# Kernel tuning notes

Hardware: AMD Instinct MI355X
Metric: run time of the kernel (lower is better)

## Reference

```python
import jax, jax.numpy as jnp
import numpy as np

B, N, DIM = 32, 576, 1024
H, HD = 16, 64            # head_dim = DIM // H
M = HD * 2                # rand_feat_dim = head_dim * rand_feat_dim_ratio(2) = 128
LAM = 0.1
NUM_STEP = 10
SCALE = HD ** (-0.5)


def setup_inputs() -> dict:
    key = jax.random.key(0)
    ks = jax.random.split(key, 6)
    x = jax.random.normal(ks[0], (B, N, DIM), dtype=jnp.float32)
    qkv_w = jax.random.normal(ks[1], (2 * DIM, DIM), dtype=jnp.float32) * 0.02
    proj_w = jax.random.normal(ks[2], (DIM, DIM), dtype=jnp.float32) * 0.02
    proj_b = jnp.zeros((DIM,), dtype=jnp.float32)
    rand_matrix = jax.random.normal(ks[3], (H, HD, M), dtype=jnp.float32)
    kernel = jax.random.normal(ks[4], (1, H, N, M), dtype=jnp.float32)
    learned_k = jnp.eye(2 * M, dtype=jnp.float32)
    learned_lam = jnp.ones((1,), dtype=jnp.float32)
    learned_L = jnp.ones((1,), dtype=jnp.float32)
    return {"x": x, "qkv_w": qkv_w, "proj_w": proj_w, "proj_b": proj_b,
            "rand_matrix": rand_matrix, "kernel": kernel,
            "learned_k": learned_k, "learned_lam": learned_lam,
            "learned_L": learned_L}


def _soft_thresh(z, t):
    # torch: sign(z) * GELU(|z| - t), exact (erf) GELU
    return jnp.sign(z) * jax.nn.gelu(jnp.abs(z) - t, approximate=False)


def reference(x, qkv_w, proj_w, proj_b, rand_matrix, kernel,
              learned_k, learned_lam, learned_L):
    # qkv projection (no bias), split into q and v heads: [B,H,N,HD]
    qkv = (x @ qkv_w.T).reshape(B, N, 2, H, HD)
    q = jnp.transpose(qkv[:, :, 0], (0, 2, 1, 3))
    v = jnp.transpose(qkv[:, :, 1], (0, 2, 1, 3))

    # random-feature map (Performer-style positive features)
    q = q * SCALE ** 0.5
    logits = jnp.einsum('bhnd,hdm->bhnm', q, rand_matrix)
    sqnorm = 0.5 * jnp.sum(q * q, axis=-1, keepdims=True)
    phi = jnp.exp(logits - sqnorm) / (M ** 0.5)                 # [B,H,N,M]

    # concat learned kernel features, L2-normalize over token dim (dim=-2)
    q = jnp.concatenate([phi, jnp.broadcast_to(kernel, (B, H, N, M))], axis=-1)
    nrm = jnp.linalg.norm(q, axis=-2, keepdims=True)
    q = q / jnp.maximum(nrm, 1e-12)                              # [B,H,N,2M]

    kk = jnp.einsum('bhnp,bhnq->bhpq', q, q)                     # [B,H,2M,2M]
    inp = jnp.einsum('bhnp,bhnd->bhpd', q, v)                    # [B,H,2M,HD]

    # ISTA-like unrolled solver
    L = jax.lax.stop_gradient(
        jnp.max(jnp.sum(jnp.abs(kk), axis=-1), axis=-1))[..., None, None] + 1.0
    lam_learned = learned_lam * LAM                              # [1]
    eff_L = L / learned_L                                        # [B,H,1,1]
    kk_learned = jnp.einsum('pq,bhqr,rs->bhps', learned_k, kk, learned_k)

    z = _soft_thresh(inp, lam_learned)
    for _ in range(NUM_STEP):
        z = z - (jnp.einsum('bhpq,bhqd->bhpd', kk_learned, z) - inp) / eff_L
        z = _soft_thresh(z, lam_learned / eff_L)

    out = jnp.einsum('bhnp,bhpd->bhnd', q, z)                    # [B,H,N,HD]
    out = jnp.transpose(out, (0, 2, 1, 3)).reshape(B, N, DIM)
    return out @ proj_w.T + proj_b
```

## Files before the change

kernel.cpp:

```cpp
#include <hip/hip_runtime.h>
#include <math.h>

#define NN 576
#define LAMC 0.1f
#define NUM_STEP 10

typedef unsigned short u16;
typedef __attribute__((ext_vector_type(8))) short bf16x8;
typedef __attribute__((ext_vector_type(4))) float f32x4;

__device__ __forceinline__ float bf2f(u16 u) { return __uint_as_float(((unsigned)u) << 16); }
__device__ __forceinline__ u16 f2bf(float f) {
    unsigned x = __float_as_uint(f);
    return (u16)((x + 0x7fffu + ((x >> 16) & 1u)) >> 16);
}
__device__ __forceinline__ float soft_thresh(float z, float t) {
    float a = fabsf(z) - t;
    float g = 0.5f * a * (1.0f + erff(a * 0.70710678118654752f));
    float s = (z > 0.0f) ? 1.0f : ((z < 0.0f) ? -1.0f : 0.0f);
    return s * g;
}
__device__ __forceinline__ void gload16(const u16* g, const u16* l) {
    __builtin_amdgcn_global_load_lds(
        (const __attribute__((address_space(1))) unsigned int*)(g),
        (__attribute__((address_space(3))) unsigned int*)(l), 16, 0, 0);
}

__global__ __launch_bounds__(256) void k_prep(const float* __restrict__ x,
                                              const float* __restrict__ qkv_w,
                                              const float* __restrict__ proj_w,
                                              const float* __restrict__ Lk,
                                              const float* __restrict__ rand_m,
                                              const float* __restrict__ kern,
                                              u16* __restrict__ xb,
                                              u16* __restrict__ wb,
                                              u16* __restrict__ pwb,
                                              u16* __restrict__ Lkb,
                                              u16* __restrict__ LkTb,
                                              u16* __restrict__ randT,
                                              u16* __restrict__ kerT) {
    const int b = blockIdx.x;
    if (b < 18432) {
        const int i = b * 256 + threadIdx.x;
        float4 v = reinterpret_cast<const float4*>(x)[i];
        ushort4 o; o.x = f2bf(v.x); o.y = f2bf(v.y); o.z = f2bf(v.z); o.w = f2bf(v.w);
        reinterpret_cast<ushort4*>(xb)[i] = o;
    } else if (b < 20480) {
        const int i = (b - 18432) * 256 + threadIdx.x;
        float4 v = reinterpret_cast<const float4*>(qkv_w)[i];
        ushort4 o; o.x = f2bf(v.x); o.y = f2bf(v.y); o.z = f2bf(v.z); o.w = f2bf(v.w);
        reinterpret_cast<ushort4*>(wb)[i] = o;
    } else if (b < 21504) {
        const int i = (b - 20480) * 256 + threadIdx.x;
        float4 v = reinterpret_cast<const float4*>(proj_w)[i];
        ushort4 o; o.x = f2bf(v.x); o.y = f2bf(v.y); o.z = f2bf(v.z); o.w = f2bf(v.w);
        reinterpret_cast<ushort4*>(pwb)[i] = o;
    } else if (b < 21568) {
        const int i = (b - 21504) * 256 + threadIdx.x;
        float4 v = reinterpret_cast<const float4*>(Lk)[i];
        ushort4 o; o.x = f2bf(v.x); o.y = f2bf(v.y); o.z = f2bf(v.z); o.w = f2bf(v.w);
        reinterpret_cast<ushort4*>(Lkb)[i] = o;
    } else if (b < 21824) {
        const int r = b - 21568, s = threadIdx.x;
        LkTb[r * 256 + s] = f2bf(Lk[s * 256 + r]);
    } else if (b < 22336) {
        const int i = (b - 21824) * 256 + threadIdx.x;
        const int h = i >> 13, rem = i & 8191;
        const int m = rem >> 6, d = rem & 63;
        randT[i] = f2bf(rand_m[(size_t)h * 8192 + d * 128 + m]);
    } else {
        const int h = b - 22336, m = threadIdx.x;
        if (m < 128) {
            const float* kp = kern + (size_t)h * NN * 128 + m;
            float s = 0.f;
            for (int n = 0; n < NN; ++n) { float v = kp[(size_t)n * 128]; s = fmaf(v, v, s); }
            const float inv = 1.0f / fmaxf(sqrtf(s), 1e-12f);
            u16* op = kerT + ((size_t)h * 128 + m) * 576;
            for (int n = 0; n < NN; ++n) op[n] = f2bf(kp[(size_t)n * 128] * inv);
        }
    }
}

__device__ __forceinline__ void nt128_k64(const u16* __restrict__ A, const u16* __restrict__ B,
                                          const int K, u16 (&As)[128][64], u16 (&Bs)[128][64],
                                          f32x4 (&acc)[4][4]) {
    const int tid = threadIdx.x;
    const int lane = tid & 63, wid = tid >> 6;
    const int wr = (wid >> 1) * 64, wc = (wid & 1) * 64;
    const int fr = lane & 15, kg = lane >> 4;
    const int lrow = lane >> 3;
    const int lslot = (lane & 7) ^ ((lane >> 3) & 7);
    for (int k0 = 0; k0 < K; k0 += 64) {
        __syncthreads();
        #pragma unroll
        for (int c = 0; c < 4; ++c) {
            const int ch = wid + c * 4;
            gload16(&A[(size_t)(ch * 8 + lrow) * K + k0 + lslot * 8], &As[ch * 8][0]);
            gload16(&B[(size_t)(ch * 8 + lrow) * K + k0 + lslot * 8], &Bs[ch * 8][0]);
        }
        __syncthreads();
        #pragma unroll
        for (int ks = 0; ks < 2; ++ks) {
            const int rs = ((ks * 4 + kg) ^ (fr & 7)) * 8;
            bf16x8 af[4], bfr[4];
            #pragma unroll
            for (int i = 0; i < 4; ++i) af[i] = *reinterpret_cast<const bf16x8*>(&As[wr + i * 16 + fr][rs]);
            #pragma unroll
            for (int j = 0; j < 4; ++j) bfr[j] = *reinterpret_cast<const bf16x8*>(&Bs[wc + j * 16 + fr][rs]);
            #pragma unroll
            for (int i = 0; i < 4; ++i)
                #pragma unroll
                for (int j = 0; j < 4; ++j)
                    acc[i][j] = __builtin_amdgcn_mfma_f32_16x16x32_bf16(af[i], bfr[j], acc[i][j], 0, 0, 0);
        }
    }
}

__global__ __launch_bounds__(256) void k_qkv_mfma(const u16* __restrict__ A,
                                                  const u16* __restrict__ B,
                                                  u16* __restrict__ qbf,
                                                  u16* __restrict__ vT) {
    __shared__ u16 As[128][64];
    __shared__ u16 Bs[128][64];
    const int tid = threadIdx.x;
    const int wid = tid >> 6, lane = tid & 63;
    const int wr = (wid >> 1) * 64, wc = (wid & 1) * 64;
    const int lb = (blockIdx.x & 7) * 288 + (blockIdx.x >> 3);
    const int bm = lb >> 4, bn = lb & 15;
    const int row0 = bm * 128, col0 = bn * 128;
    const int fr = lane & 15, kg = lane >> 4;
    f32x4 acc[4][4];
    #pragma unroll
    for (int i = 0; i < 4; ++i)
        #pragma unroll
        for (int j = 0; j < 4; ++j) acc[i][j] = (f32x4){0.f, 0.f, 0.f, 0.f};
    nt128_k64(A + (size_t)row0 * 1024, B + (size_t)col0 * 1024, 1024, As, Bs, acc);
    const bool isQ = (col0 < 1024);
    if (isQ) {
        const float qscale = 0.35355339059327373f;
        #pragma unroll
        for (int i = 0; i < 4; ++i) {
            #pragma unroll
            for (int r = 0; r < 4; ++r) {
                const int grow = row0 + wr + i * 16 + kg * 4 + r;
                const int b = grow / NN, n = grow % NN;
                #pragma unroll
                for (int j = 0; j < 4; ++j) {
                    const int gcol = col0 + wc + j * 16 + fr;
                    const int h = gcol >> 6, d = gcol & 63;
                    qbf[(((size_t)b * 16 + h) * NN + n) * 64 + d] = f2bf(acc[i][j][r] * qscale);
                }
            }
        }
    } else {
        #pragma unroll
        for (int i = 0; i < 4; ++i) {
            const int gb = row0 + wr + i * 16 + kg * 4;
            const int b = gb / NN, n = gb % NN;
            #pragma unroll
            for (int j = 0; j < 4; ++j) {
                const int c2 = col0 + wc + j * 16 + fr - 1024;
                const int h = c2 >> 6, d = c2 & 63;
                ushort4 pk;
                pk.x = f2bf(acc[i][j][0]); pk.y = f2bf(acc[i][j][1]);
                pk.z = f2bf(acc[i][j][2]); pk.w = f2bf(acc[i][j][3]);
                *reinterpret_cast<ushort4*>(&vT[(((size_t)b * 16 + h) * 64 + d) * 576 + n]) = pk;
            }
        }
    }
}

__global__ __launch_bounds__(256) void k_phi_mfma(const u16* __restrict__ qbf,
                                                  const u16* __restrict__ randT,
                                                  u16* __restrict__ phiT,
                                                  float* __restrict__ invn) {
    __shared__ u16 Rs[128][72];
    __shared__ u16 Qs[64][72];
    __shared__ u16 Ph[128][72];
    __shared__ float sn[64];
    __shared__ float snorm[256];
    const int bh = blockIdx.x, h = bh & 15;
    const int tid = threadIdx.x, lane = tid & 63, wid = tid >> 6;
    const int fr = lane & 15, kg = lane >> 4;
    #pragma unroll
    for (int c = 0; c < 4; ++c) {
        const int i = c * 256 + tid;
        const int m = i >> 3, k8 = (i & 7) * 8;
        *reinterpret_cast<uint4*>(&Rs[m][k8]) =
            *reinterpret_cast<const uint4*>(&randT[((size_t)h * 128 + m) * 64 + k8]);
    }
    const u16* Q = qbf + (size_t)bh * 576 * 64;
    const float invM = 0.08838834764831845f;
    float accs = 0.f;
    const int m2 = tid >> 1, c0 = (tid & 1) * 32;
    for (int nc = 0; nc < 9; ++nc) {
        const int n0 = nc * 64;
        __syncthreads();
        #pragma unroll
        for (int c = 0; c < 2; ++c) {
            const int i = c * 256 + tid;
            const int r = i >> 3, k8 = (i & 7) * 8;
            *reinterpret_cast<uint4*>(&Qs[r][k8]) =
                *reinterpret_cast<const uint4*>(&Q[(size_t)(n0 + r) * 64 + k8]);
        }
        __syncthreads();
        if (tid < 64) {
            float s = 0.f;
            #pragma unroll 8
            for (int d = 0; d < 64; ++d) { float v = bf2f(Qs[tid][d]); s = fmaf(v, v, s); }
            sn[tid] = 0.5f * s;
        }
        f32x4 acc[2][4];
        #pragma unroll
        for (int i = 0; i < 2; ++i)
            #pragma unroll
            for (int j = 0; j < 4; ++j) acc[i][j] = (f32x4){0.f, 0.f, 0.f, 0.f};
        #pragma unroll
        for (int ks = 0; ks < 2; ++ks) {
            bf16x8 af[2], bq[4];
            #pragma unroll
            for (int i = 0; i < 2; ++i)
                af[i] = *reinterpret_cast<const bf16x8*>(&Rs[wid * 32 + i * 16 + fr][ks * 32 + kg * 8]);
            #pragma unroll
            for (int j = 0; j < 4; ++j)
                bq[j] = *reinterpret_cast<const bf16x8*>(&Qs[j * 16 + fr][ks * 32 + kg * 8]);
            #pragma unroll
            for (int i = 0; i < 2; ++i)
                #pragma unroll
                for (int j = 0; j < 4; ++j)
                    acc[i][j] = __builtin_amdgcn_mfma_f32_16x16x32_bf16(af[i], bq[j], acc[i][j], 0, 0, 0);
        }
        __syncthreads();
        #pragma unroll
        for (int j = 0; j < 4; ++j) {
            const int n = j * 16 + fr;
            const float sv = sn[n];
            #pragma unroll
            for (int i = 0; i < 2; ++i) {
                #pragma unroll
                for (int r = 0; r < 4; ++r) {
                    const int m = wid * 32 + i * 16 + kg * 4 + r;
                    Ph[m][n] = f2bf(expf(acc[i][j][r] - sv) * invM);
                }
            }
        }
        __syncthreads();
        #pragma unroll
        for (int c = 0; c < 4; ++c) {
            const int i = c * 256 + tid;
            const int mm = i >> 3, k8 = (i & 7) * 8;
            *reinterpret_cast<uint4*>(&phiT[((size_t)bh * 128 + mm) * 576 + n0 + k8]) =
                *reinterpret_cast<const uint4*>(&Ph[mm][k8]);
        }
        {
            float s = 0.f;
            #pragma unroll 8
            for (int t = 0; t < 32; ++t) { float v = bf2f(Ph[m2][c0 + t]); s = fmaf(v, v, s); }
            accs += s;
        }
    }
    snorm[tid] = accs;
    __syncthreads();
    if (tid < 128)
        invn[bh * 128 + tid] = 1.0f / fmaxf(sqrtf(snorm[tid * 2] + snorm[tid * 2 + 1]), 1e-12f);
}

__global__ __launch_bounds__(512, 2) void k_gram_fat(const u16* __restrict__ phiT,
                                                     const u16* __restrict__ kerT,
                                                     const float* __restrict__ invn,
                                                     const float* __restrict__ lL,
                                                     u16* __restrict__ kkb,
                                                     float* __restrict__ effL) {
    __shared__ u16 Qs[256][64];
    __shared__ float rs2[2][256];
    __shared__ float red[256];
    const int bh = blockIdx.x, h = bh & 15;
    const int tid = threadIdx.x, lane = tid & 63, wid = tid >> 6;
    const int wr = (wid & 3) * 64, wc = (wid >> 2) * 128;
    const int fr = lane & 15, kg = lane >> 4;
    const int lrow = lane >> 3;
    const int lslot = (lane & 7) ^ ((lane >> 3) & 7);
    f32x4 acc[4][8];
    #pragma unroll
    for (int i = 0; i < 4; ++i)
        #pragma unroll
        for (int j = 0; j < 8; ++j) acc[i][j] = (f32x4){0.f, 0.f, 0.f, 0.f};
    for (int k0 = 0; k0 < 576; k0 += 64) {
        __syncthreads();
        #pragma unroll
        for (int c = 0; c < 4; ++c) {
            const int rowbase = (wid * 4 + c) * 8;
            const int p = rowbase + lrow;
            const u16* src = (p < 128)
                ? phiT + ((size_t)bh * 128 + p) * 576 + k0 + lslot * 8
                : kerT + ((size_t)h * 128 + (p - 128)) * 576 + k0 + lslot * 8;
            gload16(src, &Qs[rowbase][0]);
        }
        __syncthreads();
        #pragma unroll
        for (int ks = 0; ks < 2; ++ks) {
            const int rs = ((ks * 4 + kg) ^ (fr & 7)) * 8;
            bf16x8 af[4], bf[8];
            #pragma unroll
            for (int i = 0; i < 4; ++i) af[i] = *reinterpret_cast<const bf16x8*>(&Qs[wr + i * 16 + fr][rs]);
            #pragma unroll
            for (int j = 0; j < 8; ++j) bf[j] = *reinterpret_cast<const bf16x8*>(&Qs[wc + j * 16 + fr][rs]);
            #pragma unroll
            for (int i = 0; i < 4; ++i)
                #pragma unroll
                for (int j = 0; j < 8; ++j)
                    acc[i][j] = __builtin_amdgcn_mfma_f32_16x16x32_bf16(af[i], bf[j], acc[i][j], 0, 0, 0);
        }
    }
    const float* iv = invn + bh * 128;
    u16* C = kkb + (size_t)bh * 65536;
    float sq[8];
    #pragma unroll
    for (int j = 0; j < 8; ++j) { const int q = wc + j * 16 + fr; sq[j] = (q < 128) ? iv[q] : 1.0f; }
    #pragma unroll
    for (int i = 0; i < 4; ++i)
        #pragma unroll
        for (int rr = 0; rr < 4; ++rr) {
            const int p = wr + i * 16 + kg * 4 + rr;
            const float sp = (p < 128) ? iv[p] : 1.0f;
            float rsum = 0.f;
            #pragma unroll
            for (int j = 0; j < 8; ++j) {
                const float val = acc[i][j][rr] * sp * sq[j];
                C[(size_t)p * 256 + wc + j * 16 + fr] = f2bf(val);
                rsum += fabsf(val);
            }
            #pragma unroll
            for (int mk = 1; mk < 16; mk <<= 1) rsum += __shfl_xor(rsum, mk);
            if (fr == 0) rs2[wid >> 2][p] = rsum;
        }
    __syncthreads();
    if (tid < 256) red[tid] = rs2[0][tid] + rs2[1][tid];
    __syncthreads();
    for (int st = 128; st > 0; st >>= 1) {
        if (tid < st) red[tid] = fmaxf(red[tid], red[tid + st]);
        __syncthreads();
    }
    if (tid == 0) effL[bh] = (red[0] + 1.0f) / lL[0];
}

__global__ __launch_bounds__(512, 2) void k_lk_fat(const u16* __restrict__ Ab, size_t sA,
                                                   const u16* __restrict__ Bb, size_t sB,
                                                   u16* __restrict__ Cb) {
    __shared__ u16 As[256][64];
    __shared__ u16 Bs[256][64];
    const int idx = blockIdx.x;
    const int tid = threadIdx.x, lane = tid & 63, wid = tid >> 6;
    const int wr = (wid & 3) * 64, wc = (wid >> 2) * 128;
    const int fr = lane & 15, kg = lane >> 4;
    const int lrow = lane >> 3;
    const int lslot = (lane & 7) ^ ((lane >> 3) & 7);
    const u16* A = Ab + (size_t)idx * sA;
    const u16* B = Bb + (size_t)idx * sB;
    f32x4 acc[4][8];
    #pragma unroll
    for (int i = 0; i < 4; ++i)
        #pragma unroll
        for (int j = 0; j < 8; ++j) acc[i][j] = (f32x4){0.f, 0.f, 0.f, 0.f};
    for (int k0 = 0; k0 < 256; k0 += 64) {
        __syncthreads();
        #pragma unroll
        for (int c = 0; c < 4; ++c) {
            const int rowbase = (wid * 4 + c) * 8;
            const int p = rowbase + lrow;
            gload16(&A[(size_t)p * 256 + k0 + lslot * 8], &As[rowbase][0]);
            gload16(&B[(size_t)p * 256 + k0 + lslot * 8], &Bs[rowbase][0]);
        }
        __syncthreads();
        #pragma unroll
        for (int ks = 0; ks < 2; ++ks) {
            const int rs = ((ks * 4 + kg) ^ (fr & 7)) * 8;
            bf16x8 af[4], bf[8];
            #pragma unroll
            for (int i = 0; i < 4; ++i) af[i] = *reinterpret_cast<const bf16x8*>(&As[wr + i * 16 + fr][rs]);
            #pragma unroll
            for (int j = 0; j < 8; ++j) bf[j] = *reinterpret_cast<const bf16x8*>(&Bs[wc + j * 16 + fr][rs]);
            #pragma unroll
            for (int i = 0; i < 4; ++i)
                #pragma unroll
                for (int j = 0; j < 8; ++j)
                    acc[i][j] = __builtin_amdgcn_mfma_f32_16x16x32_bf16(af[i], bf[j], acc[i][j], 0, 0, 0);
        }
    }
    u16* C = Cb + (size_t)idx * 65536;
    #pragma unroll
    for (int i = 0; i < 4; ++i)
        #pragma unroll
        for (int rr = 0; rr < 4; ++rr) {
            const int p = wr + i * 16 + kg * 4 + rr;
            #pragma unroll
            for (int j = 0; j < 8; ++j)
                C[(size_t)p * 256 + wc + j * 16 + fr] = f2bf(acc[i][j][rr]);
        }
}

__global__ __launch_bounds__(256) void k_inp_mfma(const u16* __restrict__ vT,
                                                  const u16* __restrict__ phiT,
                                                  const u16* __restrict__ kerT,
                                                  const float* __restrict__ invn,
                                                  float* __restrict__ inpT) {
    __shared__ u16 As[64][32];
    __shared__ u16 Bs[256][32];
    const int bh = blockIdx.x, h = bh & 15;
    const int tid = threadIdx.x, lane = tid & 63, wid = tid >> 6;
    const int fr = lane & 15, kg = lane >> 4;
    const int lrow = lane >> 2;
    const int lslot = (lane & 3) ^ ((lane >> 3) & 3);
    const u16* Av = vT + (size_t)bh * 64 * 576;
    f32x4 acc[4][4];
    #pragma unroll
    for (int i = 0; i < 4; ++i)
        #pragma unroll
        for (int j = 0; j < 4; ++j) acc[i][j] = (f32x4){0.f, 0.f, 0.f, 0.f};
    const int rslot = (kg ^ ((fr >> 1) & 3)) * 8;
    for (int k0 = 0; k0 < 576; k0 += 32) {
        __syncthreads();
        gload16(&Av[(size_t)(wid * 16 + lrow) * 576 + k0 + lslot * 8], &As[wid * 16][0]);
        #pragma unroll
        for (int c = 0; c < 4; ++c) {
            const int chunk = wid + c * 4;
            const int p = chunk * 16 + lrow;
            const u16* src = (p < 128)
                ? phiT + ((size_t)bh * 128 + p) * 576 + k0 + lslot * 8
                : kerT + ((size_t)h * 128 + (p - 128)) * 576 + k0 + lslot * 8;
            gload16(src, &Bs[chunk * 16][0]);
        }
        __syncthreads();
        bf16x8 af[4], bfr[4];
        #pragma unroll
        for (int i = 0; i < 4; ++i) af[i] = *reinterpret_cast<const bf16x8*>(&As[i * 16 + fr][rslot]);
        #pragma unroll
        for (int j = 0; j < 4; ++j) bfr[j] = *reinterpret_cast<const bf16x8*>(&Bs[wid * 64 + j * 16 + fr][rslot]);
        #pragma unroll
        for (int i = 0; i < 4; ++i)
            #pragma unroll
            for (int j = 0; j < 4; ++j)
                acc[i][j] = __builtin_amdgcn_mfma_f32_16x16x32_bf16(af[i], bfr[j], acc[i][j], 0, 0, 0);
    }
    float* O = inpT + (size_t)bh * 16384;
    float sc[4];
    #pragma unroll
    for (int j = 0; j < 4; ++j) {
        const int p = wid * 64 + j * 16 + fr;
        sc[j] = (p < 128) ? invn[bh * 128 + p] : 1.0f;
    }
    #pragma unroll
    for (int i = 0; i < 4; ++i)
        #pragma unroll
        for (int r = 0; r < 4; ++r)
            #pragma unroll
            for (int j = 0; j < 4; ++j)
                O[(size_t)(i * 16 + kg * 4 + r) * 256 + wid * 64 + j * 16 + fr] = acc[i][j][r] * sc[j];
}

__global__ __launch_bounds__(256) void k_ista_reg(const u16* __restrict__ kkl,
                                                  const float* __restrict__ inpT,
                                                  u16* __restrict__ zbf,
                                                  const float* __restrict__ effL,
                                                  const float* __restrict__ llam) {
    __shared__ u16 zs[32][256];
    const int lb = (blockIdx.x & 7) * 128 + (blockIdx.x >> 3);
    const int bh = lb >> 1, dh = lb & 1;
    const int tid = threadIdx.x, lane = tid & 63, wid = tid >> 6;
    const int wr = wid * 64;
    const int fr = lane & 15, kg = lane >> 4;
    const u16* Kk = kkl + (size_t)bh * 65536;
    bf16x8 af[4][8];
    #pragma unroll
    for (int i = 0; i < 4; ++i) {
        const int p = wr + i * 16 + fr;
        #pragma unroll
        for (int c = 0; c < 8; ++c)
            af[i][c] = *reinterpret_cast<const bf16x8*>(&Kk[(size_t)p * 256 + c * 32 + kg * 8]);
    }
    const float* I = inpT + (size_t)bh * 16384 + (size_t)dh * 32 * 256;
    const float invL = 1.0f / effL[bh];
    const float lam = llam[0] * LAMC;
    const float thr = lam * invL;
    float4 ip[4][2];
    #pragma unroll
    for (int i = 0; i < 4; ++i) {
        const int pb = wr + i * 16 + kg * 4;
        #pragma unroll
        for (int j = 0; j < 2; ++j) {
            const int d = j * 16 + fr;
            ip[i][j] = *reinterpret_cast<const float4*>(&I[(size_t)d * 256 + pb]);
            const int pc = pb ^ ((d & 7) << 3);
            ushort4 pk;
            pk.x = f2bf(soft_thresh(ip[i][j].x, lam));
            pk.y = f2bf(soft_thresh(ip[i][j].y, lam));
            pk.z = f2bf(soft_thresh(ip[i][j].z, lam));
            pk.w = f2bf(soft_thresh(ip[i][j].w, lam));
            *reinterpret_cast<ushort4*>(&zs[d][pc]) = pk;
        }
    }
    __syncthreads();
    for (int step = 0; step < NUM_STEP; ++step) {
        f32x4 acc[4][2];
        #pragma unroll
        for (int i = 0; i < 4; ++i)
            #pragma unroll
            for (int j = 0; j < 2; ++j) acc[i][j] = (f32x4){0.f, 0.f, 0.f, 0.f};
        #pragma unroll
        for (int c = 0; c < 8; ++c) {
            bf16x8 bz[2];
            #pragma unroll
            for (int j = 0; j < 2; ++j) {
                const int d = j * 16 + fr;
                bz[j] = *reinterpret_cast<const bf16x8*>(&zs[d][(c * 32 + kg * 8) ^ ((d & 7) << 3)]);
            }
            #pragma unroll
            for (int i = 0; i < 4; ++i)
                #pragma unroll
                for (int j = 0; j < 2; ++j)
                    acc[i][j] = __builtin_amdgcn_mfma_f32_16x16x32_bf16(af[i][c], bz[j], acc[i][j], 0, 0, 0);
        }
        __syncthreads();
        #pragma unroll
        for (int i = 0; i < 4; ++i) {
            const int pb = wr + i * 16 + kg * 4;
            #pragma unroll
            for (int j = 0; j < 2; ++j) {
                const int d = j * 16 + fr;
                const int pc = pb ^ ((d & 7) << 3);
                ushort4 zo = *reinterpret_cast<const ushort4*>(&zs[d][pc]);
                ushort4 pk;
                pk.x = f2bf(soft_thresh(bf2f(zo.x) - (acc[i][j][0] - ip[i][j].x) * invL, thr));
                pk.y = f2bf(soft_thresh(bf2f(zo.y) - (acc[i][j][1] - ip[i][j].y) * invL, thr));
                pk.z = f2bf(soft_thresh(bf2f(zo.z) - (acc[i][j][2] - ip[i][j].z) * invL, thr));
                pk.w = f2bf(soft_thresh(bf2f(zo.w) - (acc[i][j][3] - ip[i][j].w) * invL, thr));
                *reinterpret_cast<ushort4*>(&zs[d][pc]) = pk;
            }
        }
        __syncthreads();
    }
    u16* Z = zbf + (size_t)bh * 16384 + (size_t)dh * 32 * 256;
    #pragma unroll
    for (int c = 0; c < 4; ++c) {
        const int i = c * 256 + tid;
        const int d = i >> 5, p8 = (i & 31) * 8;
        *reinterpret_cast<uint4*>(&Z[(size_t)d * 256 + p8]) =
            *reinterpret_cast<const uint4*>(&zs[d][p8 ^ ((d & 7) << 3)]);
    }
}

__global__ __launch_bounds__(256) void k_outpre_mfma(const u16* __restrict__ phiT,
                                                     const u16* __restrict__ kerT,
                                                     const u16* __restrict__ zbf,
                                                     const float* __restrict__ invn,
                                                     u16* __restrict__ outp) {
    __shared__ u16 Zs[64][264];
    __shared__ u16 Qt[64][264];
    __shared__ u16 Os[64][72];
    const int bh = blockIdx.x, b = bh >> 4, h = bh & 15;
    const int tid = threadIdx.x, lane = tid & 63, wid = tid >> 6;
    const int fr = lane & 15, kg = lane >> 4;
    const u16* Z = zbf + (size_t)bh * 16384;
    #pragma unroll
    for (int c = 0; c < 8; ++c) {
        const int i = c * 256 + tid;
        const int d = i >> 5, k8 = (i & 31) * 8;
        uint4 v = *reinterpret_cast<const uint4*>(&Z[(size_t)d * 256 + k8]);
        if (k8 < 128) {
            const float4 s0 = *reinterpret_cast<const float4*>(&invn[bh * 128 + k8]);
            const float4 s1 = *reinterpret_cast<const float4*>(&invn[bh * 128 + k8 + 4]);
            uint4 o;
            o.x = (unsigned)f2bf(__uint_as_float(v.x << 16) * s0.x) |
                  ((unsigned)f2bf(__uint_as_float(v.x & 0xffff0000u) * s0.y) << 16);
            o.y = (unsigned)f2bf(__uint_as_float(v.y << 16) * s0.z) |
                  ((unsigned)f2bf(__uint_as_float(v.y & 0xffff0000u) * s0.w) << 16);
            o.z = (unsigned)f2bf(__uint_as_float(v.z << 16) * s1.x) |
                  ((unsigned)f2bf(__uint_as_float(v.z & 0xffff0000u) * s1.y) << 16);
            o.w = (unsigned)f2bf(__uint_as_float(v.w << 16) * s1.z) |
                  ((unsigned)f2bf(__uint_as_float(v.w & 0xffff0000u) * s1.w) << 16);
            v = o;
        }
        *reinterpret_cast<uint4*>(&Zs[d][k8]) = v;
    }
    for (int nc = 0; nc < 9; ++nc) {
        const int n0 = nc * 64;
        __syncthreads();
        #pragma unroll
        for (int c = 0; c < 8; ++c) {
            const int i = c * 256 + tid;
            const int p = i >> 3, j8 = (i & 7) * 8;
            const u16* src = (p < 128) ? &phiT[((size_t)bh * 128 + p) * 576 + n0 + j8]
                                       : &kerT[((size_t)h * 128 + (p - 128)) * 576 + n0 + j8];
            uint4 v = *reinterpret_cast<const uint4*>(src);
            Qt[j8 + 0][p] = (u16)(v.x & 0xffffu); Qt[j8 + 1][p] = (u16)(v.x >> 16);
            Qt[j8 + 2][p] = (u16)(v.y & 0xffffu); Qt[j8 + 3][p] = (u16)(v.y >> 16);
            Qt[j8 + 4][p] = (u16)(v.z & 0xffffu); Qt[j8 + 5][p] = (u16)(v.z >> 16);
            Qt[j8 + 6][p] = (u16)(v.w & 0xffffu); Qt[j8 + 7][p] = (u16)(v.w >> 16);
        }
        __syncthreads();
        f32x4 acc[4];
        #pragma unroll
        for (int j = 0; j < 4; ++j) acc[j] = (f32x4){0.f, 0.f, 0.f, 0.f};
        #pragma unroll
        for (int ks = 0; ks < 8; ++ks) {
            bf16x8 aq = *reinterpret_cast<const bf16x8*>(&Qt[wid * 16 + fr][ks * 32 + kg * 8]);
            #pragma unroll
            for (int j = 0; j < 4; ++j) {
                bf16x8 bz = *reinterpret_cast<const bf16x8*>(&Zs[j * 16 + fr][ks * 32 + kg * 8]);
                acc[j] = __builtin_amdgcn_mfma_f32_16x16x32_bf16(aq, bz, acc[j], 0, 0, 0);
            }
        }
        __syncthreads();
        #pragma unroll
        for (int j = 0; j < 4; ++j)
            #pragma unroll
            for (int r = 0; r < 4; ++r)
                Os[wid * 16 + kg * 4 + r][j * 16 + fr] = f2bf(acc[j][r]);
        __syncthreads();
        #pragma unroll
        for (int c = 0; c < 2; ++c) {
            const int i = c * 256 + tid;
            const int nn = i >> 3, k8 = (i & 7) * 8;
            *reinterpret_cast<uint4*>(&outp[((size_t)b * NN + n0 + nn) * 1024 + h * 64 + k8]) =
                *reinterpret_cast<const uint4*>(&Os[nn][k8]);
        }
    }
}

__global__ __launch_bounds__(256) void k_proj_mfma(const u16* __restrict__ A,
                                                   const u16* __restrict__ B,
                                                   const float* __restrict__ bias,
                                                   float* __restrict__ out) {
    __shared__ u16 As[128][64];
    __shared__ u16 Bs[128][64];
    const int tid = threadIdx.x;
    const int wid = tid >> 6, lane = tid & 63;
    const int wr = (wid >> 1) * 64, wc = (wid & 1) * 64;
    const int lb = (blockIdx.x & 7) * 144 + (blockIdx.x >> 3);
    const int bm = lb >> 3, bn = lb & 7;
    const int row0 = bm * 128, col0 = bn * 128;
    const int fr = lane & 15, kg = lane >> 4;
    f32x4 acc[4][4];
    #pragma unroll
    for (int i = 0; i < 4; ++i)
        #pragma unroll
        for (int j = 0; j < 4; ++j) acc[i][j] = (f32x4){0.f, 0.f, 0.f, 0.f};
    nt128_k64(A + (size_t)row0 * 1024, B + (size_t)col0 * 1024, 1024, As, Bs, acc);
    #pragma unroll
    for (int i = 0; i < 4; ++i)
        #pragma unroll
        for (int r = 0; r < 4; ++r) {
            const int grow = row0 + wr + i * 16 + kg * 4 + r;
            #pragma unroll
            for (int j = 0; j < 4; ++j) {
                const int gcol = col0 + wc + j * 16 + fr;
                out[(size_t)grow * 1024 + gcol] = acc[i][j][r] + bias[gcol];
            }
        }
}

extern "C" void kernel_launch(void* const* d_in, const int* in_sizes, int n_in,
                              void* d_out, int out_size, void* d_ws, size_t ws_size,
                              hipStream_t stream) {
    const float* x      = (const float*)d_in[0];
    const float* qkv_w  = (const float*)d_in[1];
    const float* proj_w = (const float*)d_in[2];
    const float* proj_b = (const float*)d_in[3];
    const float* rand_m = (const float*)d_in[4];
    const float* kern   = (const float*)d_in[5];
    const float* Lk     = (const float*)d_in[6];
    const float* llam   = (const float*)d_in[7];
    const float* lL     = (const float*)d_in[8];
    float* out = (float*)d_out;

    const size_t NEED = 248514560ull;
    if (ws_size < NEED) { hipMemsetAsync(d_out, 0, (size_t)out_size * 4, stream); return; }
    char* base = (char*)d_ws;
    u16*   pwb  = (u16*)  (base + 0);
    float* effL = (float*)(base + 2097152);
    u16*   Lkb  = (u16*)  (base + 2099200);
    u16*   LkTb = (u16*)  (base + 2230272);
    u16*   kerT = (u16*)  (base + 2361344);
    u16*   randT= (u16*)  (base + 4720640);
    u16*   phiT = (u16*)  (base + 4982784);
    u16*   kkb  = (u16*)  (base + 80480256);
    float* inpT = (float*)(base + 147589120);
    u16*   zbf  = (u16*)  (base + 181143552);
    float* invn = (float*)(base + 248252416);
    u16*   vT   = (u16*)  (base + 80480256);
    u16*   wb   = (u16*)  (base + 118228992);
    u16*   qbf  = (u16*)  (base + 147589120);
    u16*   xb   = (u16*)  (base + 197920768);
    u16*   tmpb = (u16*)  (base + 181143552);
    u16*   outp = (u16*)  (base + 80480256);

    k_prep       <<<22352, 256, 0, stream>>>(x, qkv_w, proj_w, Lk, rand_m, kern,
                                             xb, wb, pwb, Lkb, LkTb, randT, kerT);
    k_qkv_mfma   <<<2304,  256, 0, stream>>>(xb, wb, qbf, vT);
    k_phi_mfma   <<<512,   256, 0, stream>>>(qbf, randT, phiT, invn);
    k_inp_mfma   <<<512,   256, 0, stream>>>(vT, phiT, kerT, invn, inpT);
    k_gram_fat   <<<512,   512, 0, stream>>>(phiT, kerT, invn, lL, kkb, effL);
    k_lk_fat     <<<512,   512, 0, stream>>>(Lkb, 0, kkb, 65536, tmpb);
    k_lk_fat     <<<512,   512, 0, stream>>>(tmpb, 65536, LkTb, 0, kkb);
    k_ista_reg   <<<1024,  256, 0, stream>>>(kkb, inpT, zbf, effL, llam);
    k_outpre_mfma<<<512,   256, 0, stream>>>(phiT, kerT, zbf, invn, outp);
    k_proj_mfma  <<<1152,  256, 0, stream>>>(outp, pwb, proj_b, out);
}
```

Before: 571.3 us.

## Fuse the two learned-kernel sandwich GEMMs into one kernel; widen inp K-tile

The two back-to-back k_lk_fat launches computing Lk·kk·LkT are merged into one kernel. The intermediate 256x256 product stays in a swizzled shared-memory tile instead of going through a global temp buffer. This removes one launch and a global round trip per head, at the cost of 144KB LDS per block and occupancy of one block per CU. Separately, k_inp_mfma now uses a K tile of 64 instead of 32, which halves the number of barrier-separated load steps.

```diff
diff --git a/kernel.cpp b/kernel.cpp
--- a/kernel.cpp
+++ b/kernel.cpp
@@ -344,42 +344,91 @@
     if (tid == 0) effL[bh] = (red[0] + 1.0f) / lL[0];
 }
 
-__global__ __launch_bounds__(512, 2) void k_lk_fat(const u16* __restrict__ Ab, size_t sA,
-                                                   const u16* __restrict__ Bb, size_t sB,
-                                                   u16* __restrict__ Cb) {
-    __shared__ u16 As[256][64];
-    __shared__ u16 Bs[256][64];
-    const int idx = blockIdx.x;
+__global__ __launch_bounds__(512, 1) void k_lk_fused(const u16* __restrict__ Lkb,
+                                                     const u16* __restrict__ LkTb,
+                                                     u16* __restrict__ kkb) {
+    __shared__ u16 smem[73728];
+    u16 (*t)[256]  = reinterpret_cast<u16(*)[256]>(smem);
+    u16 (*As1)[64] = reinterpret_cast<u16(*)[64]>(smem);
+    u16 (*Bs1)[64] = reinterpret_cast<u16(*)[64]>(smem + 16384);
+    u16 (*Bs2)[32] = reinterpret_cast<u16(*)[32]>(smem + 65536);
+    const int bh = blockIdx.x;
     const int tid = threadIdx.x, lane = tid & 63, wid = tid >> 6;
     const int wr = (wid & 3) * 64, wc = (wid >> 2) * 128;
     const int fr = lane & 15, kg = lane >> 4;
-    const int lrow = lane >> 3;
-    const int lslot = (lane & 7) ^ ((lane >> 3) & 7);
-    const u16* A = Ab + (size_t)idx * sA;
-    const u16* B = Bb + (size_t)idx * sB;
+    const u16* B1 = kkb + (size_t)bh * 65536;
     f32x4 acc[4][8];
     #pragma unroll
     for (int i = 0; i < 4; ++i)
         #pragma unroll
         for (int j = 0; j < 8; ++j) acc[i][j] = (f32x4){0.f, 0.f, 0.f, 0.f};
-    for (int k0 = 0; k0 < 256; k0 += 64) {
-        __syncthreads();
-        #pragma unroll
-        for (int c = 0; c < 4; ++c) {
-            const int rowbase = (wid * 4 + c) * 8;
-            const int p = rowbase + lrow;
-            gload16(&A[(size_t)p * 256 + k0 + lslot * 8], &As[rowbase][0]);
-            gload16(&B[(size_t)p * 256 + k0 + lslot * 8], &Bs[rowbase][0]);
-        }
-        __syncthreads();
-        #pragma unroll
-        for (int ks = 0; ks < 2; ++ks) {
-            const int rs = ((ks * 4 + kg) ^ (fr & 7)) * 8;
+    {
+        const int lrow = lane >> 3;
+        const int lslot = (lane & 7) ^ ((lane >> 3) & 7);
+        for (int k0 = 0; k0 < 256; k0 += 64) {
+            __syncthreads();
+            #pragma unroll
+            for (int c = 0; c < 4; ++c) {
+                const int rowbase = (wid * 4 + c) * 8;
+                const int p = rowbase + lrow;
+                gload16(&Lkb[(size_t)p * 256 + k0 + lslot * 8], &As1[rowbase][0]);
+                gload16(&B1[(size_t)p * 256 + k0 + lslot * 8], &Bs1[rowbase][0]);
+            }
+            __syncthreads();
+            #pragma unroll
+            for (int ks = 0; ks < 2; ++ks) {
+                const int rs = ((ks * 4 + kg) ^ (fr & 7)) * 8;
+                bf16x8 af[4], bf[8];
+                #pragma unroll
+                for (int i = 0; i < 4; ++i) af[i] = *reinterpret_cast<const bf16x8*>(&As1[wr + i * 16 + fr][rs]);
+                #pragma unroll
+                for (int j = 0; j < 8; ++j) bf[j] = *reinterpret_cast<const bf16x8*>(&Bs1[wc + j * 16 + fr][rs]);
+                #pragma unroll
+                for (int i = 0; i < 4; ++i)
+                    #pragma unroll
+                    for (int j = 0; j < 8; ++j)
+                        acc[i][j] = __builtin_amdgcn_mfma_f32_16x16x32_bf16(af[i], bf[j], acc[i][j], 0, 0, 0);
+            }
+        }
+    }
+    __syncthreads();
+    #pragma unroll
+    for (int i = 0; i < 4; ++i)
+        #pragma unroll
+        for (int rr = 0; rr < 4; ++rr) {
+            const int p = wr + i * 16 + kg * 4 + rr;
+            #pragma unroll
+            for (int j = 0; j < 8; ++j) {
+                const int q = wc + j * 16 + fr;
+                t[p][q ^ ((p & 7) << 3)] = f2bf(acc[i][j][rr]);
+            }
+        }
+    __syncthreads();
+    #pragma unroll
+    for (int i = 0; i < 4; ++i)
+        #pragma unroll
+        for (int j = 0; j < 8; ++j) acc[i][j] = (f32x4){0.f, 0.f, 0.f, 0.f};
+    {
+        const int lrow2 = lane >> 2;
+        const int lslot2 = (lane & 3) ^ ((lane >> 3) & 3);
+        const int rslot2 = (kg ^ ((fr >> 1) & 3)) * 8;
+        for (int k0 = 0; k0 < 256; k0 += 32) {
+            __syncthreads();
+            #pragma unroll
+            for (int c = 0; c < 2; ++c) {
+                const int chunk = wid * 2 + c;
+                const int p = chunk * 16 + lrow2;
+                gload16(&LkTb[(size_t)p * 256 + k0 + lslot2 * 8], &Bs2[chunk * 16][0]);
+            }
+            __syncthreads();
             bf16x8 af[4], bf[8];
             #pragma unroll
-            for (int i = 0; i < 4; ++i) af[i] = *reinterpret_cast<const bf16x8*>(&As[wr + i * 16 + fr][rs]);
-            #pragma unroll
-            for (int j = 0; j < 8; ++j) bf[j] = *reinterpret_cast<const bf16x8*>(&Bs[wc + j * 16 + fr][rs]);
+            for (int i = 0; i < 4; ++i) {
+                const int p = wr + i * 16 + fr;
+                af[i] = *reinterpret_cast<const bf16x8*>(&t[p][(k0 + kg * 8) ^ ((p & 7) << 3)]);
+            }
+            #pragma unroll
+            for (int j = 0; j < 8; ++j) bf[j] = *reinterpret_cast<const bf16x8*>(&Bs2[wc + j * 16 + fr][rslot2]);
             #pragma unroll
             for (int i = 0; i < 4; ++i)
                 #pragma unroll
@@ -387,7 +436,7 @@
                     acc[i][j] = __builtin_amdgcn_mfma_f32_16x16x32_bf16(af[i], bf[j], acc[i][j], 0, 0, 0);
         }
     }
-    u16* C = Cb + (size_t)idx * 65536;
+    u16* C = kkb + (size_t)bh * 65536;
     #pragma unroll
     for (int i = 0; i < 4; ++i)
         #pragma unroll
@@ -404,43 +453,50 @@
                                                   const u16* __restrict__ kerT,
                                                   const float* __restrict__ invn,
                                                   float* __restrict__ inpT) {
-    __shared__ u16 As[64][32];
-    __shared__ u16 Bs[256][32];
+    __shared__ u16 As[64][64];
+    __shared__ u16 Bs[256][64];
     const int bh = blockIdx.x, h = bh & 15;
     const int tid = threadIdx.x, lane = tid & 63, wid = tid >> 6;
     const int fr = lane & 15, kg = lane >> 4;
-    const int lrow = lane >> 2;
-    const int lslot = (lane & 3) ^ ((lane >> 3) & 3);
+    const int lrow = lane >> 3;
+    const int lslot = (lane & 7) ^ ((lane >> 3) & 7);
     const u16* Av = vT + (size_t)bh * 64 * 576;
     f32x4 acc[4][4];
     #pragma unroll
     for (int i = 0; i < 4; ++i)
         #pragma unroll
         for (int j = 0; j < 4; ++j) acc[i][j] = (f32x4){0.f, 0.f, 0.f, 0.f};
-    const int rslot = (kg ^ ((fr >> 1) & 3)) * 8;
-    for (int k0 = 0; k0 < 576; k0 += 32) {
-        __syncthreads();
-        gload16(&Av[(size_t)(wid * 16 + lrow) * 576 + k0 + lslot * 8], &As[wid * 16][0]);
-        #pragma unroll
-        for (int c = 0; c < 4; ++c) {
+    for (int k0 = 0; k0 < 576; k0 += 64) {
+        __syncthreads();
+        #pragma unroll
+        for (int c = 0; c < 2; ++c) {
+            const int chunk = wid * 2 + c;
+            gload16(&Av[(size_t)(chunk * 8 + lrow) * 576 + k0 + lslot * 8], &As[chunk * 8][0]);
+        }
+        #pragma unroll
+        for (int c = 0; c < 8; ++c) {
             const int chunk = wid + c * 4;
-            const int p = chunk * 16 + lrow;
+            const int p = chunk * 8 + lrow;
             const u16* src = (p < 128)
                 ? phiT + ((size_t)bh * 128 + p) * 576 + k0 + lslot * 8
                 : kerT + ((size_t)h * 128 + (p - 128)) * 576 + k0 + lslot * 8;
-            gload16(src, &Bs[chunk * 16][0]);
-        }
-        __syncthreads();
-        bf16x8 af[4], bfr[4];
-        #pragma unroll
-        for (int i = 0; i < 4; ++i) af[i] = *reinterpret_cast<const bf16x8*>(&As[i * 16 + fr][rslot]);
-        #pragma unroll
-        for (int j = 0; j < 4; ++j) bfr[j] = *reinterpret_cast<const bf16x8*>(&Bs[wid * 64 + j * 16 + fr][rslot]);
-        #pragma unroll
-        for (int i = 0; i < 4; ++i)
-            #pragma unroll
-            for (int j = 0; j < 4; ++j)
-                acc[i][j] = __builtin_amdgcn_mfma_f32_16x16x32_bf16(af[i], bfr[j], acc[i][j], 0, 0, 0);
+            gload16(src, &Bs[chunk * 8][0]);
+        }
+        __syncthreads();
+        #pragma unroll
+        for (int ks = 0; ks < 2; ++ks) {
+            const int rs = ((ks * 4 + kg) ^ (fr & 7)) * 8;
+            bf16x8 af[4], bfr[4];
+            #pragma unroll
+            for (int i = 0; i < 4; ++i) af[i] = *reinterpret_cast<const bf16x8*>(&As[i * 16 + fr][rs]);
+            #pragma unroll
+            for (int j = 0; j < 4; ++j) bfr[j] = *reinterpret_cast<const bf16x8*>(&Bs[wid * 64 + j * 16 + fr][rs]);
+            #pragma unroll
+            for (int i = 0; i < 4; ++i)
+                #pragma unroll
+                for (int j = 0; j < 4; ++j)
+                    acc[i][j] = __builtin_amdgcn_mfma_f32_16x16x32_bf16(af[i], bfr[j], acc[i][j], 0, 0, 0);
+        }
     }
     float* O = inpT + (size_t)bh * 16384;
     float sc[4];
@@ -691,7 +747,6 @@
     u16*   wb   = (u16*)  (base + 118228992);
     u16*   qbf  = (u16*)  (base + 147589120);
     u16*   xb   = (u16*)  (base + 197920768);
-    u16*   tmpb = (u16*)  (base + 181143552);
     u16*   outp = (u16*)  (base + 80480256);
 
     k_prep       <<<22352, 256, 0, stream>>>(x, qkv_w, proj_w, Lk, rand_m, kern,
@@ -700,8 +755,7 @@
     k_phi_mfma   <<<512,   256, 0, stream>>>(qbf, randT, phiT, invn);
     k_inp_mfma   <<<512,   256, 0, stream>>>(vT, phiT, kerT, invn, inpT);
     k_gram_fat   <<<512,   512, 0, stream>>>(phiT, kerT, invn, lL, kkb, effL);
-    k_lk_fat     <<<512,   512, 0, stream>>>(Lkb, 0, kkb, 65536, tmpb);
-    k_lk_fat     <<<512,   512, 0, stream>>>(tmpb, 65536, LkTb, 0, kkb);
+    k_lk_fused   <<<512,   512, 0, stream>>>(Lkb, LkTb, kkb);
     k_ista_reg   <<<1024,  256, 0, stream>>>(kkb, inpT, zbf, effL, llam);
     k_outpre_mfma<<<512,   256, 0, stream>>>(phiT, kerT, zbf, invn, outp);
     k_proj_mfma  <<<1152,  256, 0, stream>>>(outp, pwb, proj_b, out);
```

Result: no change. 564.0 us (-1.3%).
